# Kernel tuning notes

Measured on AMD Instinct MI355X. Metric: run time of the kernel, lower is better.

## Reference

```python
import jax, jax.numpy as jnp
import numpy as np

B, Q, K, D, H, HD, OUT = 4, 1024, 1024, 256, 8, 32, 256


def setup_inputs() -> dict:
    key = jax.random.key(0)
    ks = jax.random.split(key, 11)
    s = 0.05  # small init scale for weights
    return {
        "q_data": jax.random.normal(ks[0], (B, Q, D), jnp.float32),
        "m_data": jax.random.normal(ks[1], (B, K, D), jnp.float32),
        "bias": jax.random.normal(ks[2], (B, 1, 1, K), jnp.float32),
        "nonbatched_bias": jax.random.normal(ks[3], (H, Q, K), jnp.float32),
        "query_w": jax.random.normal(ks[4], (D, H, HD), jnp.float32) * s,
        "key_w": jax.random.normal(ks[5], (D, H, HD), jnp.float32) * s,
        "value_w": jax.random.normal(ks[6], (D, H, HD), jnp.float32) * s,
        "gating_w": jax.random.normal(ks[7], (D, H, HD), jnp.float32) * s,
        "gating_b": jnp.ones((H, HD), jnp.float32),
        "output_w": jax.random.normal(ks[8], (H, HD, OUT), jnp.float32) * s,
        "output_b": jnp.zeros((OUT,), jnp.float32),
    }


def reference(q_data, m_data, bias, nonbatched_bias, query_w, key_w, value_w,
              gating_w, gating_b, output_w, output_b):
    key_dim = query_w.shape[-1]
    # QKV projections; queries pre-scaled by 1/sqrt(head_dim)
    q = jnp.einsum('bqa,ahc->bqhc', q_data, query_w) * key_dim ** (-0.5)
    k = jnp.einsum('bka,ahc->bkhc', m_data, key_w)
    v = jnp.einsum('bka,ahc->bkhc', m_data, value_w)
    # attention logits [b,h,q,k] plus batched and nonbatched additive biases
    logits_update = jnp.einsum('bqhc,bkhc->bhqk', q, k)
    logits = logits_update + bias + nonbatched_bias[None]
    weights = jax.nn.softmax(logits, axis=-1)
    weighted_avg = jnp.einsum('bhqk,bkhc->bqhc', weights, v)
    # sigmoid gating on the value-aggregated output
    gate = jax.nn.sigmoid(jnp.einsum('bqc,chv->bqhv', q_data, gating_w) + gating_b)
    weighted_avg = weighted_avg * gate
    output = jnp.einsum('bqhc,hco->bqo', weighted_avg, output_w) + output_b
    return (output, logits_update)
```

## Files before the change

kernel.cpp:

```cpp
#include <hip/hip_runtime.h>
#include <hip/hip_bf16.h>

#define NB 4
#define NQ 1024
#define NKS 1024
#define ND 256
#define NH 8
#define NHD 32
#define NOUT 256

typedef __attribute__((ext_vector_type(8))) short v8s;
typedef __attribute__((ext_vector_type(4))) short v4s;
typedef __attribute__((ext_vector_type(4))) float f32x4;

__global__ __launch_bounds__(256) void prep_w(
    const float* __restrict__ qw, const float* __restrict__ kw,
    const float* __restrict__ vw, const float* __restrict__ gw,
    const float* __restrict__ ow, __hip_bfloat16* __restrict__ Wt)
{
  __shared__ float tile[64][65];
  const int wb = blockIdx.x;
  const int m = wb >> 4, bx = wb & 15;
  const float* src = (m == 0) ? qw : (m == 1) ? kw : (m == 2) ? vw
                   : (m == 3) ? gw : ow;
  const float scale = (m == 0) ? 0.1767766952966369f : 1.0f;
  const int d0 = (bx >> 2) * 64, o0 = (bx & 3) * 64;
  #pragma unroll
  for (int i = 0; i < 16; ++i) {
    const int idx = threadIdx.x + i * 256;
    tile[idx >> 6][idx & 63] = src[(size_t)(d0 + (idx >> 6)) * 256 + o0 + (idx & 63)];
  }
  __syncthreads();
  __hip_bfloat16* dst = Wt + (size_t)m * 65536;
  #pragma unroll
  for (int i = 0; i < 16; ++i) {
    const int idx = threadIdx.x + i * 256;
    const int orow = idx >> 6, dc = idx & 63;
    dst[(size_t)(o0 + orow) * 256 + d0 + dc] = __float2bfloat16(tile[dc][orow] * scale);
  }
}

__global__ __launch_bounds__(256) void proj_kernel(
    const float* __restrict__ qdata, const float* __restrict__ mdata,
    const __hip_bfloat16* __restrict__ Wt, const float* __restrict__ gating_b,
    __hip_bfloat16* __restrict__ Qw, __hip_bfloat16* __restrict__ Kw,
    __hip_bfloat16* __restrict__ Vt, __hip_bfloat16* __restrict__ G)
{
  __shared__ __align__(16) __hip_bfloat16 sA[16][264];

  const int wv = threadIdx.x >> 6, lane = threadIdx.x & 63;
  const int c = lane & 15, g = lane >> 4;
  const int ctg = wv;
  const int mat = blockIdx.x & 1;
  const int r0g = (blockIdx.x >> 1) & 255;
  const int src = blockIdx.x >> 9;
  const int r0 = r0g * 16;
  const int b = r0 >> 10, pos0 = r0 & 1023;
  const f32x4 z = {0.f, 0.f, 0.f, 0.f};

  {
    const float* A = (src ? mdata : qdata) + (size_t)r0 * 256;
    const int row = threadIdx.x >> 6, col4 = (threadIdx.x & 63) * 4;
    #pragma unroll
    for (int i = 0; i < 4; ++i) {
      const f32x4 a = *(const f32x4*)(A + (size_t)(row + i * 4) * 256 + col4);
      __hip_bfloat16 t4[4];
      t4[0] = __float2bfloat16(a.x); t4[1] = __float2bfloat16(a.y);
      t4[2] = __float2bfloat16(a.z); t4[3] = __float2bfloat16(a.w);
      *(v4s*)&sA[row + i * 4][col4] = *(v4s*)t4;
    }
  }
  __syncthreads();

  v8s af[8];
  #pragma unroll
  for (int ks = 0; ks < 8; ++ks)
    af[ks] = *(const v8s*)&sA[c][ks * 32 + g * 8];

  const int widx = (src == 0) ? (mat ? 3 : 0) : (mat ? 2 : 1);
  const __hip_bfloat16* W = Wt + (size_t)widx * 65536;
  const bool swapped = (src == 1) && (mat == 1);

  f32x4 ac[4] = {z, z, z, z};
  #pragma unroll
  for (int ks = 0; ks < 8; ++ks) {
    #pragma unroll
    for (int j = 0; j < 4; ++j) {
      v8s wf = *(const v8s*)(W + (size_t)((ctg * 4 + j) * 16 + c) * 256 + ks * 32 + g * 8);
      ac[j] = swapped
        ? __builtin_amdgcn_mfma_f32_16x16x32_bf16(wf, af[ks], ac[j], 0, 0, 0)
        : __builtin_amdgcn_mfma_f32_16x16x32_bf16(af[ks], wf, ac[j], 0, 0, 0);
    }
  }

  if (src == 0 && mat == 0) {
    #pragma unroll
    for (int j = 0; j < 4; ++j) {
      const int o = (ctg * 4 + j) * 16 + c, h = o >> 5, hd = o & 31;
      #pragma unroll
      for (int r = 0; r < 4; ++r)
        Qw[((size_t)(b * NH + h) * 1024 + pos0 + 4 * g + r) * 32 + hd] =
            __float2bfloat16(ac[j][r]);
    }
  } else if (src == 0) {
    #pragma unroll
    for (int j = 0; j < 4; ++j) {
      const int o = (ctg * 4 + j) * 16 + c;
      const float gb = gating_b[o];
      #pragma unroll
      for (int r = 0; r < 4; ++r)
        G[(size_t)(r0 + 4 * g + r) * 256 + o] = __float2bfloat16(ac[j][r] + gb);
    }
  } else if (mat == 0) {
    #pragma unroll
    for (int j = 0; j < 4; ++j) {
      const int o = (ctg * 4 + j) * 16 + c, h = o >> 5, hd = o & 31;
      #pragma unroll
      for (int r = 0; r < 4; ++r)
        Kw[((size_t)(b * NH + h) * 1024 + pos0 + 4 * g + r) * 32 + hd] =
            __float2bfloat16(ac[j][r]);
    }
  } else {
    #pragma unroll
    for (int j = 0; j < 4; ++j) {
      #pragma unroll
      for (int r = 0; r < 4; ++r) {
        const int o2 = (ctg * 4 + j) * 16 + 4 * g + r;
        Vt[((size_t)(b * NH + (o2 >> 5)) * 32 + (o2 & 31)) * 1024 + pos0 + c] =
            __float2bfloat16(ac[j][r]);
      }
    }
  }
}

__global__ __launch_bounds__(256) void attn_kernel(
    const __hip_bfloat16* __restrict__ Qw, const __hip_bfloat16* __restrict__ Kw,
    const __hip_bfloat16* __restrict__ Vt,
    const float* __restrict__ bias, const float* __restrict__ nbb,
    const __hip_bfloat16* __restrict__ G,
    float* __restrict__ out_logits, __hip_bfloat16* __restrict__ WA)
{
  __shared__ __align__(16) __hip_bfloat16 sP[4][16][72];

  const int wv = threadIdx.x >> 6, lane = threadIdx.x & 63;
  const int c = lane & 15, g = lane >> 4;
  const int xcd   = blockIdx.x & 7;
  const int slot  = blockIdx.x >> 3;
  const int bh    = ((slot >> 4) << 3) | xcd;
  const int qtg   = slot & 15;
  const int qt  = qtg * 4 + wv;
  const int b = bh >> 3, h = bh & 7;
  const int q0 = qt * 16;
  const size_t bhs = (size_t)bh;

  const __hip_bfloat16* Kbase = Kw + bhs * NKS * NHD;
  const __hip_bfloat16* Vbase = Vt + bhs * NHD * NKS;
  const float* biasb = bias + (size_t)b * NKS;
  const float* nbbb  = nbb + ((size_t)h * NQ + q0) * NKS;

  const v8s qfrag = *(const v8s*)(Qw + (bhs * NQ + q0 + c) * NHD + g * 8);

  const f32x4 zacc = {0.f, 0.f, 0.f, 0.f};
  f32x4 O0 = zacc, O1 = zacc;
  float lsumL[4] = {0.f, 0.f, 0.f, 0.f};

  auto loadKV = [&](int k0, v8s* kf, v8s* vf) {
    kf[0] = *(const v8s*)(Kbase + (k0 +      c) * NHD + g * 8);
    kf[1] = *(const v8s*)(Kbase + (k0 + 16 + c) * NHD + g * 8);
    kf[2] = *(const v8s*)(Kbase + (k0 + 32 + c) * NHD + g * 8);
    kf[3] = *(const v8s*)(Kbase + (k0 + 48 + c) * NHD + g * 8);
    vf[0] = *(const v8s*)(Vbase + (     c) * NKS + k0 +      g * 8);
    vf[1] = *(const v8s*)(Vbase + (16 + c) * NKS + k0 +      g * 8);
    vf[2] = *(const v8s*)(Vbase + (     c) * NKS + k0 + 32 + g * 8);
    vf[3] = *(const v8s*)(Vbase + (16 + c) * NKS + k0 + 32 + g * 8);
  };
  auto loadBias = [&](int k0, float* bn) {
    #pragma unroll
    for (int t = 0; t < 4; ++t) {
      const float bvt = biasb[k0 + t * 16 + c];
      #pragma unroll
      for (int r = 0; r < 4; ++r)
        bn[t * 4 + r] = bvt + nbbb[(g * 4 + r) * NKS + k0 + t * 16 + c];
    }
  };

  auto compute = [&](int k0, const v8s* kf, const v8s* vf, const float* bn) {
    f32x4 S[4];
    #pragma unroll
    for (int t = 0; t < 4; ++t)
      S[t] = __builtin_amdgcn_mfma_f32_16x16x32_bf16(qfrag, kf[t], zacc, 0, 0, 0);

    #pragma unroll
    for (int r = 0; r < 4; ++r) {
      const int qrow = q0 + g * 4 + r;
      float* lp = out_logits + (bhs * NQ + qrow) * (size_t)NKS + k0 + c;
      float psum = 0.f;
      #pragma unroll
      for (int t = 0; t < 4; ++t) {
        lp[t * 16] = S[t][r];
        const float p = __expf(S[t][r] + bn[t * 4 + r]);
        psum += p;
        sP[wv][g * 4 + r][t * 16 + c] = __float2bfloat16(p);
      }
      lsumL[r] += psum;
    }

    const v8s pa0 = *(const v8s*)&sP[wv][c][g * 8];
    const v8s pa1 = *(const v8s*)&sP[wv][c][32 + g * 8];
    O0 = __builtin_amdgcn_mfma_f32_16x16x32_bf16(pa0, vf[0], O0, 0, 0, 0);
    O0 = __builtin_amdgcn_mfma_f32_16x16x32_bf16(pa1, vf[2], O0, 0, 0, 0);
    O1 = __builtin_amdgcn_mfma_f32_16x16x32_bf16(pa0, vf[1], O1, 0, 0, 0);
    O1 = __builtin_amdgcn_mfma_f32_16x16x32_bf16(pa1, vf[3], O1, 0, 0, 0);
  };

  v8s kfA[4], vfA[4], kfB[4], vfB[4];
  float bnA[16], bnB[16];

  loadKV(0, kfA, vfA);
  loadBias(0, bnA);
  #pragma unroll 1
  for (int kt = 0; kt < NKS / 64; kt += 2) {
    loadKV((kt + 1) * 64, kfB, vfB);
    loadBias((kt + 1) * 64, bnB);
    compute(kt * 64, kfA, vfA, bnA);
    if (kt + 2 < NKS / 64) {
      loadKV((kt + 2) * 64, kfA, vfA);
      loadBias((kt + 2) * 64, bnA);
    }
    compute((kt + 1) * 64, kfB, vfB, bnB);
  }

  #pragma unroll
  for (int r = 0; r < 4; ++r) {
    float rs = lsumL[r];
    rs += __shfl_xor(rs, 1);
    rs += __shfl_xor(rs, 2);
    rs += __shfl_xor(rs, 4);
    rs += __shfl_xor(rs, 8);
    const float inv = 1.0f / rs;
    const int qrow = q0 + g * 4 + r;
    const size_t gb = ((size_t)b * NQ + qrow) * 256 + h * NHD;
    const float gl0 = __bfloat162float(G[gb + c]);
    const float gl1 = __bfloat162float(G[gb + 16 + c]);
    WA[gb + c]      = __float2bfloat16(O0[r] * inv * (1.f / (1.f + __expf(-gl0))));
    WA[gb + 16 + c] = __float2bfloat16(O1[r] * inv * (1.f / (1.f + __expf(-gl1))));
  }
}

__global__ __launch_bounds__(256) void outproj_kernel(
    const __hip_bfloat16* __restrict__ WA, const __hip_bfloat16* __restrict__ WtO,
    const float* __restrict__ output_b, float* __restrict__ out)
{
  const int t = threadIdx.x;
  const int wv = t >> 6, lane = t & 63;
  const int c = lane & 15, g = lane >> 4;
  const int r0 = blockIdx.x * 16;

  const f32x4 z = {0.f, 0.f, 0.f, 0.f};
  f32x4 ac[4] = {z, z, z, z};
  #pragma unroll
  for (int ks = 0; ks < 8; ++ks) {
    const v8s af = *(const v8s*)(WA + (size_t)(r0 + c) * 256 + ks * 32 + g * 8);
    #pragma unroll
    for (int j = 0; j < 4; ++j) {
      const v8s wf = *(const v8s*)(WtO + (size_t)((wv * 4 + j) * 16 + c) * 256 + ks * 32 + g * 8);
      ac[j] = __builtin_amdgcn_mfma_f32_16x16x32_bf16(af, wf, ac[j], 0, 0, 0);
    }
  }
  #pragma unroll
  for (int j = 0; j < 4; ++j) {
    const int o = (wv * 4 + j) * 16 + c;
    const float ob = output_b[o];
    #pragma unroll
    for (int r = 0; r < 4; ++r)
      out[(size_t)(r0 + 4 * g + r) * 256 + o] = ac[j][r] + ob;
  }
}

extern "C" void kernel_launch(void* const* d_in, const int* in_sizes, int n_in,
                              void* d_out, int out_size, void* d_ws, size_t ws_size,
                              hipStream_t stream) {
  const float* q_data   = (const float*)d_in[0];
  const float* m_data   = (const float*)d_in[1];
  const float* bias     = (const float*)d_in[2];
  const float* nbb      = (const float*)d_in[3];
  const float* query_w  = (const float*)d_in[4];
  const float* key_w    = (const float*)d_in[5];
  const float* value_w  = (const float*)d_in[6];
  const float* gating_w = (const float*)d_in[7];
  const float* gating_b = (const float*)d_in[8];
  const float* output_w = (const float*)d_in[9];
  const float* output_b = (const float*)d_in[10];

  float* out        = (float*)d_out;
  float* out_logits = out + (size_t)NB * NQ * NOUT;

  char* ws = (char*)d_ws;
  const size_t MB = 1u << 20;
  __hip_bfloat16* Qw  = (__hip_bfloat16*)(ws);
  __hip_bfloat16* Kw  = (__hip_bfloat16*)(ws + 2 * MB);
  __hip_bfloat16* Vt  = (__hip_bfloat16*)(ws + 4 * MB);
  __hip_bfloat16* G   = (__hip_bfloat16*)(ws + 6 * MB);
  __hip_bfloat16* WA  = (__hip_bfloat16*)(ws + 10 * MB);
  __hip_bfloat16* Wt  = (__hip_bfloat16*)(ws + 20 * MB);

  prep_w<<<80, 256, 0, stream>>>(query_w, key_w, value_w, gating_w, output_w, Wt);
  proj_kernel<<<1024, 256, 0, stream>>>(q_data, m_data, Wt, gating_b, Qw, Kw, Vt, G);
  attn_kernel<<<512, 256, 0, stream>>>(Qw, Kw, Vt, bias, nbb, G, out_logits, WA);
  outproj_kernel<<<256, 256, 0, stream>>>(WA, Wt + (size_t)4 * 65536, output_b, out);
}
```

Baseline: 76.26 us.

## Split logits output writes into separate high-parallelism kernel

Moves the fp32 logits_update store out of the fused attention kernel into a new logits_kernel launched with 2048 blocks that recomputes QK^T and writes the 128MB-scale logits tensor. The attention kernel then only does softmax and PV, so its long serial k-loop is no longer burdened by large global stores. This costs a second QK^T computation, an extra launch, and serialization, since the two kernels now run back to back instead of overlapping the write traffic with compute.

Measured after the change: 90.27 us. +18.4%, slower.

```diff
diff --git a/kernel.cpp b/kernel.cpp
--- a/kernel.cpp
+++ b/kernel.cpp
@@ -133,12 +133,56 @@
   }
 }
 
+__global__ __launch_bounds__(256) void logits_kernel(
+    const __hip_bfloat16* __restrict__ Qw, const __hip_bfloat16* __restrict__ Kw,
+    float* __restrict__ out_logits)
+{
+  const int wv = threadIdx.x >> 6, lane = threadIdx.x & 63;
+  const int c = lane & 15, g = lane >> 4;
+  const int xcd   = blockIdx.x & 7;
+  const int slot  = blockIdx.x >> 3;
+  const int bh    = ((slot >> 6) << 3) | xcd;
+  const int inner = slot & 63;
+  const int sp    = inner >> 4;
+  const int qtg   = inner & 15;
+  const int qt  = qtg * 4 + wv;
+  const int q0 = qt * 16;
+  const int kbase = sp * 256;
+  const size_t bhs = (size_t)bh;
+
+  const __hip_bfloat16* Kbase = Kw + bhs * NKS * NHD;
+  const v8s qfrag = *(const v8s*)(Qw + (bhs * NQ + q0 + c) * NHD + g * 8);
+  const f32x4 zacc = {0.f, 0.f, 0.f, 0.f};
+
+  #pragma unroll
+  for (int kt = 0; kt < 4; ++kt) {
+    const int k0 = kbase + kt * 64;
+    v8s kf[4];
+    kf[0] = *(const v8s*)(Kbase + (k0 +      c) * NHD + g * 8);
+    kf[1] = *(const v8s*)(Kbase + (k0 + 16 + c) * NHD + g * 8);
+    kf[2] = *(const v8s*)(Kbase + (k0 + 32 + c) * NHD + g * 8);
+    kf[3] = *(const v8s*)(Kbase + (k0 + 48 + c) * NHD + g * 8);
+
+    f32x4 S[4];
+    #pragma unroll
+    for (int t = 0; t < 4; ++t)
+      S[t] = __builtin_amdgcn_mfma_f32_16x16x32_bf16(qfrag, kf[t], zacc, 0, 0, 0);
+
+    #pragma unroll
+    for (int r = 0; r < 4; ++r) {
+      float* lp = out_logits + (bhs * NQ + q0 + g * 4 + r) * (size_t)NKS + k0 + c;
+      #pragma unroll
+      for (int t = 0; t < 4; ++t)
+        lp[t * 16] = S[t][r];
+    }
+  }
+}
+
 __global__ __launch_bounds__(256) void attn_kernel(
     const __hip_bfloat16* __restrict__ Qw, const __hip_bfloat16* __restrict__ Kw,
     const __hip_bfloat16* __restrict__ Vt,
     const float* __restrict__ bias, const float* __restrict__ nbb,
-    const __hip_bfloat16* __restrict__ G,
-    float* __restrict__ out_logits, __hip_bfloat16* __restrict__ WA)
+    const __hip_bfloat16* __restrict__ G, __hip_bfloat16* __restrict__ WA)
 {
   __shared__ __align__(16) __hip_bfloat16 sP[4][16][72];
 
@@ -192,12 +236,9 @@
 
     #pragma unroll
     for (int r = 0; r < 4; ++r) {
-      const int qrow = q0 + g * 4 + r;
-      float* lp = out_logits + (bhs * NQ + qrow) * (size_t)NKS + k0 + c;
       float psum = 0.f;
       #pragma unroll
       for (int t = 0; t < 4; ++t) {
-        lp[t * 16] = S[t][r];
         const float p = __expf(S[t][r] + bn[t * 4 + r]);
         psum += p;
         sP[wv][g * 4 + r][t * 16 + c] = __float2bfloat16(p);
@@ -306,6 +347,7 @@
 
   prep_w<<<80, 256, 0, stream>>>(query_w, key_w, value_w, gating_w, output_w, Wt);
   proj_kernel<<<1024, 256, 0, stream>>>(q_data, m_data, Wt, gating_b, Qw, Kw, Vt, G);
-  attn_kernel<<<512, 256, 0, stream>>>(Qw, Kw, Vt, bias, nbb, G, out_logits, WA);
+  logits_kernel<<<2048, 256, 0, stream>>>(Qw, Kw, out_logits);
+  attn_kernel<<<512, 256, 0, stream>>>(Qw, Kw, Vt, bias, nbb, G, WA);
   outproj_kernel<<<256, 256, 0, stream>>>(WA, Wt + (size_t)4 * 65536, output_b, out);
 }
```
